# Performance work log

Measured on AMD Instinct MI355X. Metric: run time of the kernel, lower is better.

## Reference

```python
import jax, jax.numpy as jnp
import numpy as np
import math

MIN_NORM = 1e-15
EPS = 1e-7
MAX_NORM = 1e6

N = 100000      # num nodes (aaa)
E = 1600000     # num edges
D_IN = 129      # embedding_num (1 time coord + 128 spatial)
D_OUT = 128     # output1_dim
MAXLEN = 50
B = 4096
NCLASS = 5

# ---------------- Hyperboloid manifold ops (HGCN-style) ----------------

def proj(x, c):
    K = 1. / c
    y = x[..., 1:]
    y_sq = jnp.sum(y * y, axis=-1, keepdims=True)
    x0 = jnp.sqrt(jnp.clip(K + y_sq, EPS))
    return jnp.concatenate([x0, y], axis=-1)

def proj_tan0(u, c):
    # zero out the time coordinate
    return jnp.concatenate([jnp.zeros_like(u[..., :1]), u[..., 1:]], axis=-1)

def expmap0(u, c):
    K = 1. / c
    sqrtK = jnp.sqrt(K)
    x = u[..., 1:]
    xn = jnp.maximum(jnp.linalg.norm(x, axis=-1, keepdims=True), MIN_NORM)
    theta = xn / sqrtK
    first = sqrtK * jnp.cosh(theta)
    rest = sqrtK * jnp.sinh(theta) * x / xn
    return proj(jnp.concatenate([first, rest], axis=-1), c)

def logmap0(x, c):
    K = 1. / c
    sqrtK = jnp.sqrt(K)
    y = x[..., 1:]
    yn = jnp.maximum(jnp.linalg.norm(y, axis=-1, keepdims=True), MIN_NORM)
    theta = jnp.clip(x[..., 0:1] / sqrtK, 1.0 + EPS)
    rest = sqrtK * jnp.arccosh(theta) * y / yn
    return jnp.concatenate([jnp.zeros_like(theta), rest], axis=-1)

def minkowski_dot(x, y):
    return jnp.sum(x * y, axis=-1, keepdims=True) - 2.0 * x[..., 0:1] * y[..., 0:1]

def minkowski_norm(u):
    return jnp.sqrt(jnp.clip(minkowski_dot(u, u), EPS))

def expmap(u, x, c):
    K = 1. / c
    sqrtK = jnp.sqrt(K)
    normu = jnp.minimum(minkowski_norm(u), MAX_NORM)
    theta = jnp.maximum(normu / sqrtK, MIN_NORM)
    result = jnp.cosh(theta) * x + jnp.sinh(theta) * u / theta
    return proj(result, c)

def proj_tan(u, x, c):
    ux = jnp.sum(x[..., 1:] * u[..., 1:], axis=-1, keepdims=True)
    vals0 = ux / jnp.clip(x[..., 0:1], EPS)
    return jnp.concatenate([vals0, u[..., 1:]], axis=-1)

def ptransp0(x, u, c):
    K = 1. / c
    sqrtK = jnp.sqrt(K)
    x0 = x[..., 0:1]
    y = x[..., 1:]
    yn = jnp.maximum(jnp.linalg.norm(y, axis=-1, keepdims=True), MIN_NORM)
    yhat = y / yn
    v = jnp.concatenate([-yn, (sqrtK - x0) * yhat], axis=-1)
    alpha = jnp.sum(yhat * u[..., 1:], axis=-1, keepdims=True) / sqrtK
    return proj_tan(u - alpha * v, x, c)

def mobius_add(x, y, c):
    u = logmap0(y, c)
    v = ptransp0(x, jnp.broadcast_to(u, x.shape), c)
    return expmap(v, x, c)

def mobius_add0(x, y, c):
    # tangent-space addition at the origin
    return expmap0(logmap0(x, c) + logmap0(y, c), c)

def mobius_matvec1(m, x, c):
    return expmap0(logmap0(x, c) @ m, c)

def mobius_matvec0(n, x, c):
    # per-row scalar mobius scaling (n is (N,1))
    return expmap0(n * logmap0(x, c), c)

def hyp_bias_point(b, c):
    return proj(expmap0(proj_tan0(b[None, :], c), c), c)

def gcn_layer(x, w, b, rows, cols, vals, c, n_nodes):
    out = mobius_matvec1(w, x, c)
    out = mobius_add(out, hyp_bias_point(b, c), c)
    out = logmap0(out, c)
    out = jax.ops.segment_sum(vals[:, None] * out[cols], rows, num_segments=n_nodes)
    return proj(expmap0(out, c), c)


def setup_inputs() -> dict:
    key = jax.random.key(0)
    ks = jax.random.split(key, 20)
    def ku(k, shape, fan_in):
        bound = 1.0 / math.sqrt(fan_in)
        return jax.random.uniform(k, shape, jnp.float32, -bound, bound)
    inp = {}
    inp['A1_tensor'] = jax.random.normal(ks[0], (N, D_IN), jnp.float32)
    inp['adj_rows'] = jax.random.randint(ks[1], (E,), 0, N)
    inp['adj_cols'] = jax.random.randint(ks[2], (E,), 0, N)
    inp['adj_vals'] = jax.random.uniform(ks[3], (E,), jnp.float32) * 0.1
    inp['batch_idx'] = jax.random.randint(ks[4], (B, 1, MAXLEN), 0, N)
    inp['raw_c'] = jnp.array([math.log(math.exp(1.0) - 1.0)], jnp.float32)
    inp['n_param'] = jax.random.uniform(ks[5], (N, 1), jnp.float32)
    inp['Lin1'] = ku(ks[6], (D_IN, D_OUT), D_IN)
    inp['Lin1_bias'] = ku(ks[7], (D_OUT,), D_IN)
    inp['gc1_w'] = ku(ks[8], (D_IN, D_OUT), D_IN)
    inp['gc1_b'] = ku(ks[9], (D_OUT,), D_IN)
    inp['gc2_w'] = ku(ks[10], (D_OUT, D_OUT), D_OUT)
    inp['gc2_b'] = ku(ks[11], (D_OUT,), D_OUT)
    inp['weight'] = ku(ks[12], (D_OUT, MAXLEN), D_OUT)
    inp['weight2'] = ku(ks[13], (D_OUT, MAXLEN), D_OUT)
    inp['conv1_w'] = ku(ks[14], (MAXLEN,), MAXLEN)
    inp['conv1_b'] = ku(ks[15], (1,), MAXLEN)
    inp['conv2_w'] = ku(ks[16], (MAXLEN,), MAXLEN)
    inp['conv2_b'] = ku(ks[17], (1,), MAXLEN)
    inp['classifier'] = ku(ks[18], (2 * MAXLEN, NCLASS), 2 * MAXLEN)
    inp['classifier_bias'] = ku(ks[19], (NCLASS,), 2 * MAXLEN)
    return inp


def reference(A1_tensor, adj_rows, adj_cols, adj_vals, batch_idx, raw_c, n_param,
              Lin1, Lin1_bias, gc1_w, gc1_b, gc2_w, gc2_b, weight, weight2,
              conv1_w, conv1_b, conv2_w, conv2_b, classifier, classifier_bias):
    c = jax.nn.softplus(raw_c)[0] + 1e-5
    bi = batch_idx[:, 0, :]                       # (B, L)
    flat = bi.reshape(-1)

    x_tan = proj_tan0(A1_tensor, c)
    a = proj(expmap0(x_tan, c), c)                # (N, D_IN)

    a1 = mobius_matvec1(Lin1, a, c)               # (N, D_OUT)
    a1 = mobius_add(a1, hyp_bias_point(Lin1_bias, c), c)
    a2 = mobius_matvec0(n_param, a1, c)

    x_1 = gcn_layer(a, gc1_w, gc1_b, adj_rows, adj_cols, adj_vals, c, N)
    x_1 = mobius_matvec0(1.0 - n_param, x_1, c)
    x_1 = mobius_add0(x_1, a2, c)
    x_2 = gcn_layer(x_1, gc2_w, gc2_b, adj_rows, adj_cols, adj_vals, c, N)

    # readout branch 1: x_2 gathered on batch indices
    s2 = logmap0(x_2[flat].reshape(bi.shape[0], bi.shape[1], D_OUT), c)  # (B,L,D)
    s2 = jnp.einsum('bld,dt->blt', s2, weight)    # (B, L, MAXLEN)
    s2 = jnp.einsum('blt,l->bt', s2, conv1_w) + conv1_b  # kernel-size-1 conv over channels

    # readout branch 2: a1 gathered on batch indices
    s3 = logmap0(a1[flat].reshape(bi.shape[0], bi.shape[1], D_OUT), c)
    s3 = jnp.einsum('bld,dt->blt', s3, weight2)
    s3 = jnp.einsum('blt,l->bt', s3, conv2_w) + conv2_b

    sel = jnp.concatenate([s2, s3], axis=1)       # (B, 2*MAXLEN)
    pre = sel @ classifier + classifier_bias      # (B, NCLASS)
    return jnp.argmax(pre, axis=-1), sel
```

## Files before the change

kernel.cpp:

```cpp
#include <hip/hip_runtime.h>
#include <math.h>


typedef unsigned short ushort_t;
typedef __attribute__((ext_vector_type(8))) short short8;
typedef __attribute__((ext_vector_type(4))) float f32x4;

__device__ __forceinline__ float wsum(float x){
  x += __shfl_xor(x, 32);
  x += __shfl_xor(x, 16);
  x += __shfl_xor(x, 8);
  x += __shfl_xor(x, 4);
  x += __shfl_xor(x, 2);
  x += __shfl_xor(x, 1);
  return x;
}

__device__ __forceinline__ void get_c(const float* rc, float& K, float& sK){
  float c = log1pf(expf(rc[0])) + 1e-5f;
  K  = 1.0f / c;
  sK = sqrtf(K);
}

__device__ __forceinline__ float sinhx_over_x(float x){
  if (x > 1e-3f){
    float e  = __expf(x);
    float em = __builtin_amdgcn_rcpf(e);
    return 0.5f*(e - em) * __builtin_amdgcn_rcpf(x);
  }
  return 1.0f + x*x*(1.0f/6.0f);
}

__device__ __forceinline__ float facosh(float x){
  return __logf(x + sqrtf(fmaxf(fmaf(x, x, -1.0f), 0.0f)));
}

__device__ __forceinline__ ushort_t bf16_rne(float x){
  unsigned int u = __float_as_uint(x);
  u += 0x7fffu + ((u >> 16) & 1u);
  return (ushort_t)(u >> 16);
}
__device__ __forceinline__ float bf2f(ushort_t h){
  return __uint_as_float(((unsigned int)h) << 16);
}
__device__ __forceinline__ unsigned int pack_bf16(float x, float y){
  unsigned int bx = __float_as_uint(x);
  unsigned int by = __float_as_uint(y);
  bx = (bx + 0x7fffu + ((bx >> 16) & 1u)) >> 16;
  by = (by + 0x7fffu + ((by >> 16) & 1u)) & 0xffff0000u;
  return bx | by;
}
__device__ __forceinline__ float bf_lo(unsigned int p){ return __uint_as_float(p << 16); }
__device__ __forceinline__ float bf_hi(unsigned int p){ return __uint_as_float(p & 0xffff0000u); }

__device__ __forceinline__ void chain_scalars(float tt, float tu, float uu,
                                              float K, float sK,
                                              float& At, float& Au){
  float xn  = fmaxf(sqrtf(tt), 1e-15f);
  float th  = xn / sK;
  float f   = sinhx_over_x(th);
  float pn2 = f*f*tt;
  float p0  = sqrtf(fmaxf(K + pn2, 1e-7f));
  float S_yu = f * tu;
  float yn  = fmaxf(sqrtf(pn2), 1e-15f);
  float inv_yn = __builtin_amdgcn_rcpf(yn);
  float alpha = S_yu * inv_yn / sK;
  float coef  = alpha * (sK - p0);
  float cy  = coef * inv_yn;
  float cyf = cy * f;
  float pdw  = S_yu - cy*pn2;
  float spsq = uu - 2.f*cy*S_yu + cy*cy*pn2;
  float w0 = pdw / fmaxf(p0, 1e-7f);
  float md = spsq - w0*w0;
  float normu = fminf(sqrtf(fmaxf(md, 1e-7f)), 1e6f);
  float th2 = fmaxf(normu / sK, 1e-15f);
  float e  = __expf(th2);
  float em = __builtin_amdgcn_rcpf(e);
  float ch = 0.5f*(e + em);
  float g  = (th2 > 1e-3f) ? 0.5f*(e - em)*__builtin_amdgcn_rcpf(th2)
                           : 1.0f + th2*th2*(1.0f/6.0f);
  float rn2 = ch*ch*pn2 + 2.f*ch*g*pdw + g*g*spsq;
  float r0 = sqrtf(fmaxf(K + rn2, 1e-7f));
  float ynf = fmaxf(sqrtf(rn2), 1e-15f);
  float thf = fmaxf(r0/sK, 1.f+1e-7f);
  float rf = sK * facosh(thf) * __builtin_amdgcn_rcpf(ynf);
  At = rf*(ch*f - g*cyf);
  Au = rf*g;
}

__global__ __launch_bounds__(256) void stage_a(const float* __restrict__ A1,
                                               ushort_t* __restrict__ Lhi,
                                               ushort_t* __restrict__ Llo,
                                               int* __restrict__ cnt,
                                               const float* __restrict__ b0,
                                               const float* __restrict__ b1,
                                               const float* __restrict__ b2,
                                               float* __restrict__ uu3, int n){
  size_t i = (size_t)blockIdx.x * 256 + threadIdx.x;
  size_t total = (size_t)n * 128;
  if (i < total){
    size_t row = i >> 7; int j = (int)(i & 127);
    float v = A1[row*129 + 1 + j];
    ushort_t h = bf16_rne(v);
    Lhi[i] = h;
    Llo[i] = bf16_rne(v - bf2f(h));
  }
  if (i < (size_t)n) cnt[i] = 0;
  if (blockIdx.x == 0 && threadIdx.x < 64){
    int lane = threadIdx.x;
    const float* bs[3] = {b0, b1, b2};
    for (int k = 0; k < 3; ++k){
      float x = lane ? bs[k][2*lane] : 0.0f;
      float y = bs[k][2*lane+1];
      float s = wsum(x*x + y*y);
      if (lane == 0) uu3[k] = s;
    }
  }
}

__global__ __launch_bounds__(256) void split_w(const float* __restrict__ W,
                                               ushort_t* __restrict__ Whi,
                                               ushort_t* __restrict__ Wlo){
  int id = blockIdx.x * 256 + threadIdx.x;
  int k = id >> 7, nn = id & 127;
  float v = W[(size_t)k*128 + nn];
  ushort_t h = bf16_rne(v);
  Whi[(size_t)nn*128 + k] = h;
  Wlo[(size_t)nn*128 + k] = bf16_rne(v - bf2f(h));
}

__global__ __launch_bounds__(256) void mfma_chain(const ushort_t* __restrict__ Ahi,
                                                  const ushort_t* __restrict__ Alo,
                                                  const ushort_t* __restrict__ Whi,
                                                  const ushort_t* __restrict__ Wlo,
                                                  const float* __restrict__ bias,
                                                  const float* __restrict__ uu3, int uuidx,
                                                  const float* __restrict__ raw_c,
                                                  float* __restrict__ outF,
                                                  unsigned int* __restrict__ outH,
                                                  int mode, int n, int nWaves){
  __shared__ ushort_t Wsh[2][128*128];
  int tid = threadIdx.x;
  {
    const uint4* gh = (const uint4*)Whi;
    const uint4* gl = (const uint4*)Wlo;
    uint4* sh = (uint4*)Wsh[0];
    uint4* sl = (uint4*)Wsh[1];
    #pragma unroll
    for (int i = 0; i < 8; ++i){ sh[tid + 256*i] = gh[tid + 256*i]; }
    #pragma unroll
    for (int i = 0; i < 8; ++i){ sl[tid + 256*i] = gl[tid + 256*i]; }
  }
  __syncthreads();

  int lane = tid & 63;
  int c = lane & 15, quad = lane >> 4;
  int wid = blockIdx.x * 4 + (tid >> 6);
  int nStrips = (n + 15) >> 4;

  float K, sK; get_c(raw_c, K, sK);
  float uu = uu3[uuidx];
  float uv[8];
  #pragma unroll
  for (int t = 0; t < 8; ++t){
    int col = t*16 + c;
    uv[t] = (col == 0) ? 0.f : bias[col];
  }

  for (int strip = wid; strip < nStrips; strip += nWaves){
    int m0 = strip * 16;
    int ra = m0 + c; if (ra > n - 1) ra = n - 1;
    short8 ahi[4], alo[4];
    #pragma unroll
    for (int kc = 0; kc < 4; ++kc){
      size_t aoff = (size_t)ra*128 + kc*32 + quad*8;
      ahi[kc] = *(const short8*)&Ahi[aoff];
      alo[kc] = *(const short8*)&Alo[aoff];
    }

    f32x4 acc[8];
    #pragma unroll
    for (int t = 0; t < 8; ++t){
      f32x4 z = {0.f, 0.f, 0.f, 0.f};
      acc[t] = z;
      int wrow = (t*16 + c) * 128;
      #pragma unroll
      for (int kc = 0; kc < 4; ++kc){
        int woff = wrow + kc*32 + quad*8;
        short8 bhi = *(const short8*)&Wsh[0][woff];
        short8 blo = *(const short8*)&Wsh[1][woff];
        acc[t] = __builtin_amdgcn_mfma_f32_16x16x32_bf16(ahi[kc], bhi, acc[t], 0, 0, 0);
        acc[t] = __builtin_amdgcn_mfma_f32_16x16x32_bf16(ahi[kc], blo, acc[t], 0, 0, 0);
        acc[t] = __builtin_amdgcn_mfma_f32_16x16x32_bf16(alo[kc], bhi, acc[t], 0, 0, 0);
      }
    }

    if (c == 0){
      f32x4 z = {0.f, 0.f, 0.f, 0.f};
      acc[0] = z;
    }
    #pragma unroll
    for (int r = 0; r < 4; ++r){
      float tt = 0.f, tu = 0.f;
      #pragma unroll
      for (int t = 0; t < 8; ++t){
        float v = acc[t][r];
        tt = fmaf(v, v, tt);
        tu = fmaf(v, uv[t], tu);
      }
      #pragma unroll
      for (int m = 1; m <= 8; m <<= 1){
        tt += __shfl_xor(tt, m);
        tu += __shfl_xor(tu, m);
      }
      float At, Au; chain_scalars(tt, tu, uu, K, sK, At, Au);
      int row = m0 + quad*4 + r;
      if (mode == 0){
        if (row < n){
          #pragma unroll
          for (int t = 0; t < 8; ++t){
            float o = fmaf(At, acc[t][r], Au*uv[t]);
            outF[(size_t)row*128 + t*16 + c] = o;
          }
        }
      } else {
        #pragma unroll
        for (int t = 0; t < 8; ++t){
          float o  = fmaf(At, acc[t][r], Au*uv[t]);
          float on = __shfl_xor(o, 1);
          if (row < n && !(c & 1))
            outH[(size_t)row*64 + t*8 + (c >> 1)] = pack_bf16(o, on);
        }
      }
    }
  }
}

__global__ __launch_bounds__(256) void hist_k(const int* __restrict__ rows,
                                              int* __restrict__ cnt,
                                              int* __restrict__ rnk, int e){
  int base = (blockIdx.x * 256 + threadIdx.x) * 4;
  if (base + 3 < e){
    int4 r = *(const int4*)&rows[base];
    int k0 = atomicAdd(&cnt[r.x], 1);
    int k1 = atomicAdd(&cnt[r.y], 1);
    int k2 = atomicAdd(&cnt[r.z], 1);
    int k3 = atomicAdd(&cnt[r.w], 1);
    *(int4*)&rnk[base] = make_int4(k0, k1, k2, k3);
  } else {
    for (int i = base; i < e; ++i) rnk[i] = atomicAdd(&cnt[rows[i]], 1);
  }
}

#define SCAN_ITEMS 4
__global__ __launch_bounds__(256) void scan1(const int* __restrict__ cnt,
                                             int* __restrict__ off,
                                             int* __restrict__ bsum, int n){
  __shared__ int sh[256];
  int tid = threadIdx.x;
  int base = blockIdx.x * 256 * SCAN_ITEMS + tid * SCAN_ITEMS;
  int v[SCAN_ITEMS]; int s = 0;
  #pragma unroll
  for (int i = 0; i < SCAN_ITEMS; ++i){ int idx = base+i; v[i] = (idx < n) ? cnt[idx] : 0; s += v[i]; }
  sh[tid] = s; __syncthreads();
  for (int o = 1; o < 256; o <<= 1){
    int t = (tid >= o) ? sh[tid - o] : 0; __syncthreads();
    sh[tid] += t; __syncthreads();
  }
  int excl = sh[tid] - s;
  if (tid == 255) bsum[blockIdx.x] = sh[tid];
  int run = excl;
  #pragma unroll
  for (int i = 0; i < SCAN_ITEMS; ++i){ int idx = base+i; if (idx < n) off[idx] = run; run += v[i]; }
}

__global__ void scan2(int* bsum, int G){
  if (threadIdx.x == 0 && blockIdx.x == 0){
    int run = 0;
    for (int i = 0; i < G; ++i){ int t = bsum[i]; bsum[i] = run; run += t; }
  }
}

__global__ void scan3(int* __restrict__ off, const int* __restrict__ bsum, int n){
  int i = blockIdx.x * blockDim.x + threadIdx.x;
  if (i < n) off[i] += bsum[i / (256*SCAN_ITEMS)];
}

__global__ __launch_bounds__(256) void fill_k(const int* __restrict__ rows,
                                              const int* __restrict__ cols,
                                              const float* __restrict__ vals,
                                              const int* __restrict__ off,
                                              const int* __restrict__ rnk,
                                              int2* __restrict__ ecv, int e){
  int base = (blockIdx.x * 256 + threadIdx.x) * 4;
  if (base + 3 < e){
    int4   r = *(const int4*)&rows[base];
    int4   q = *(const int4*)&rnk[base];
    int4   c = *(const int4*)&cols[base];
    float4 v = *(const float4*)&vals[base];
    int o0 = off[r.x], o1 = off[r.y], o2 = off[r.z], o3 = off[r.w];
    ecv[o0 + q.x] = make_int2(c.x, __float_as_int(v.x));
    ecv[o1 + q.y] = make_int2(c.y, __float_as_int(v.y));
    ecv[o2 + q.z] = make_int2(c.z, __float_as_int(v.z));
    ecv[o3 + q.w] = make_int2(c.w, __float_as_int(v.w));
  } else {
    for (int i = base; i < e; ++i)
      ecv[off[rows[i]] + rnk[i]] = make_int2(cols[i], __float_as_int(vals[i]));
  }
}

__device__ __forceinline__ float2 seg_gather_bf16(const unsigned int* __restrict__ h,
                                                  const int* __restrict__ off,
                                                  const int* __restrict__ cnt,
                                                  const int2* __restrict__ ecv,
                                                  int row, int lane){
  float ax = 0.f, ay = 0.f, bx = 0.f, by = 0.f;
  int st = off[row], deg = cnt[row];
  const unsigned int* __restrict__ hb = h + lane;
  for (int b = 0; b < deg; b += 64){
    int k = b + lane;
    int cc = 0; float vv = 0.f;
    if (k < deg){ int2 e = ecv[st+k]; cc = e.x; vv = __int_as_float(e.y); }
    int m = min(64, deg - b);
    for (int j = 0; j < m; j += 8){
      int   c0=__shfl(cc,j+0), c1=__shfl(cc,j+1), c2=__shfl(cc,j+2), c3=__shfl(cc,j+3);
      int   c4=__shfl(cc,j+4), c5=__shfl(cc,j+5), c6=__shfl(cc,j+6), c7=__shfl(cc,j+7);
      float v0=__shfl(vv,j+0), v1=__shfl(vv,j+1), v2=__shfl(vv,j+2), v3=__shfl(vv,j+3);
      float v4=__shfl(vv,j+4), v5=__shfl(vv,j+5), v6=__shfl(vv,j+6), v7=__shfl(vv,j+7);
      unsigned int p0 = hb[(size_t)c0*64];
      unsigned int p1 = hb[(size_t)c1*64];
      unsigned int p2 = hb[(size_t)c2*64];
      unsigned int p3 = hb[(size_t)c3*64];
      unsigned int p4 = hb[(size_t)c4*64];
      unsigned int p5 = hb[(size_t)c5*64];
      unsigned int p6 = hb[(size_t)c6*64];
      unsigned int p7 = hb[(size_t)c7*64];
      ax = fmaf(v0, bf_lo(p0), ax); ay = fmaf(v0, bf_hi(p0), ay);
      bx = fmaf(v1, bf_lo(p1), bx); by = fmaf(v1, bf_hi(p1), by);
      ax = fmaf(v2, bf_lo(p2), ax); ay = fmaf(v2, bf_hi(p2), ay);
      bx = fmaf(v3, bf_lo(p3), bx); by = fmaf(v3, bf_hi(p3), by);
      ax = fmaf(v4, bf_lo(p4), ax); ay = fmaf(v4, bf_hi(p4), ay);
      bx = fmaf(v5, bf_lo(p5), bx); by = fmaf(v5, bf_hi(p5), by);
      ax = fmaf(v6, bf_lo(p6), ax); ay = fmaf(v6, bf_hi(p6), ay);
      bx = fmaf(v7, bf_lo(p7), bx); by = fmaf(v7, bf_hi(p7), by);
    }
  }
  return make_float2(ax + bx, ay + by);
}

__global__ __launch_bounds__(256) void seg_x1(const unsigned int* __restrict__ h1,
                                              const int* __restrict__ off,
                                              const int* __restrict__ cnt,
                                              const int2* __restrict__ ecv,
                                              const float* __restrict__ loga1,
                                              const float* __restrict__ nparam,
                                              unsigned int* __restrict__ X1hi,
                                              unsigned int* __restrict__ X1lo, int n){
  int row  = (int)((blockIdx.x * blockDim.x + threadIdx.x) >> 6);
  int lane = threadIdx.x & 63;
  if (row >= n) return;
  float2 acc = seg_gather_bf16(h1, off, cnt, ecv, row, lane);
  float nv = nparam[row];
  float2 la1 = *(const float2*)&loga1[(size_t)row*128 + 2*lane];
  float ox = (1.f-nv)*acc.x + nv*la1.x;
  float oy = (1.f-nv)*acc.y + nv*la1.y;
  unsigned int hp = pack_bf16(ox, oy);
  X1hi[(size_t)row*64 + lane] = hp;
  X1lo[(size_t)row*64 + lane] = pack_bf16(ox - bf_lo(hp), oy - bf_hi(hp));
}

__global__ __launch_bounds__(256) void seg_x2(const unsigned int* __restrict__ h2,
                                              const int* __restrict__ off,
                                              const int* __restrict__ cnt,
                                              const int2* __restrict__ ecv,
                                              float* __restrict__ Lx2, int n){
  int row  = (int)((blockIdx.x * blockDim.x + threadIdx.x) >> 6);
  int lane = threadIdx.x & 63;
  if (row >= n) return;
  float2 acc = seg_gather_bf16(h2, off, cnt, ecv, row, lane);
  *(float2*)&Lx2[(size_t)row*128 + 2*lane] = acc;
}

__global__ __launch_bounds__(128) void batch_head(const float* __restrict__ Lx2,
                                                  const float* __restrict__ loga1,
                                                  const int* __restrict__ bidx,
                                                  const float* __restrict__ weight,
                                                  const float* __restrict__ weight2,
                                                  const float* __restrict__ c1w,
                                                  const float* __restrict__ c1b,
                                                  const float* __restrict__ c2w,
                                                  const float* __restrict__ c2b,
                                                  const float* __restrict__ cls,
                                                  const float* __restrict__ clsb,
                                                  float* __restrict__ out, int Bn){
  __shared__ float sg2[128], sg3[128], ssel[100], spre[5];
  __shared__ int sbi[50];
  __shared__ float sc1[50], sc2[50];
  int b = blockIdx.x, d = threadIdx.x;
  const int* bi = bidx + (size_t)b * 50;
  if (d < 50){ sbi[d] = bi[d]; sc1[d] = c1w[d]; sc2[d] = c2w[d]; }
  __syncthreads();
  int lane = d & 63;
  bool lo = d < 64;
  const float* __restrict__ tab = lo ? Lx2 : loga1;
  const float* __restrict__ cw = lo ? sc1 : sc2;
  float gx = 0.f, gy = 0.f;
  const float2* __restrict__ t2 = (const float2*)tab + lane;
  #pragma unroll
  for (int l = 0; l < 50; l += 5){
    int i0 = sbi[l+0], i1 = sbi[l+1], i2 = sbi[l+2], i3 = sbi[l+3], i4 = sbi[l+4];
    float2 p0 = t2[(size_t)i0*64];
    float2 p1 = t2[(size_t)i1*64];
    float2 p2 = t2[(size_t)i2*64];
    float2 p3 = t2[(size_t)i3*64];
    float2 p4 = t2[(size_t)i4*64];
    float w0 = cw[l+0], w1 = cw[l+1], w2 = cw[l+2], w3 = cw[l+3], w4 = cw[l+4];
    gx = fmaf(w0, p0.x, gx); gy = fmaf(w0, p0.y, gy);
    gx = fmaf(w1, p1.x, gx); gy = fmaf(w1, p1.y, gy);
    gx = fmaf(w2, p2.x, gx); gy = fmaf(w2, p2.y, gy);
    gx = fmaf(w3, p3.x, gx); gy = fmaf(w3, p3.y, gy);
    gx = fmaf(w4, p4.x, gx); gy = fmaf(w4, p4.y, gy);
  }
  if (lo){ sg2[2*lane] = gx; sg2[2*lane+1] = gy; }
  else   { sg3[2*lane] = gx; sg3[2*lane+1] = gy; }
  __syncthreads();
  if (d < 50){
    float s = 0.f;
    for (int k = 0; k < 128; ++k) s = fmaf(sg2[k], weight[k*50 + d], s);
    s += c1b[0];
    ssel[d] = s;
    out[(size_t)Bn + (size_t)b*100 + d] = s;
  } else if (d >= 64 && d < 114){
    int t = d - 64;
    float s = 0.f;
    for (int k = 0; k < 128; ++k) s = fmaf(sg3[k], weight2[k*50 + t], s);
    s += c2b[0];
    ssel[50 + t] = s;
    out[(size_t)Bn + (size_t)b*100 + 50 + t] = s;
  }
  __syncthreads();
  if (d < 5){
    float s = clsb[d];
    for (int j = 0; j < 100; ++j) s = fmaf(ssel[j], cls[j*5 + d], s);
    spre[d] = s;
  }
  __syncthreads();
  if (d == 0){
    int best = 0; float bv = spre[0];
    #pragma unroll
    for (int k = 1; k < 5; ++k) if (spre[k] > bv){ bv = spre[k]; best = k; }
    out[b] = (float)best;
  }
}

extern "C" void kernel_launch(void* const* d_in, const int* in_sizes, int n_in,
                              void* d_out, int out_size, void* d_ws, size_t ws_size,
                              hipStream_t stream) {
  const float* A1     = (const float*)d_in[0];
  const int*   rows   = (const int*)  d_in[1];
  const int*   cols   = (const int*)  d_in[2];
  const float* vals   = (const float*)d_in[3];
  const int*   bidx   = (const int*)  d_in[4];
  const float* raw_c  = (const float*)d_in[5];
  const float* nparam = (const float*)d_in[6];
  const float* Lin1   = (const float*)d_in[7];
  const float* Lin1_b = (const float*)d_in[8];
  const float* gc1_w  = (const float*)d_in[9];
  const float* gc1_b  = (const float*)d_in[10];
  const float* gc2_w  = (const float*)d_in[11];
  const float* gc2_b  = (const float*)d_in[12];
  const float* weight = (const float*)d_in[13];
  const float* weight2= (const float*)d_in[14];
  const float* c1w    = (const float*)d_in[15];
  const float* c1b    = (const float*)d_in[16];
  const float* c2w    = (const float*)d_in[17];
  const float* c2b    = (const float*)d_in[18];
  const float* cls    = (const float*)d_in[19];
  const float* clsb   = (const float*)d_in[20];

  int N  = in_sizes[0] / 129;
  int E  = in_sizes[1];
  int Bn = in_sizes[4] / 50;
  size_t NF = (size_t)N * 128;

  ushort_t* Lhi = (ushort_t*)d_ws;
  ushort_t* Llo = Lhi + NF;
  float*    S0  = (float*)d_ws;
  float*    S3  = (float*)(Llo + NF);
  unsigned int* Hb   = (unsigned int*)(S3 + NF);
  unsigned int* X1hi = Hb + NF/2;
  unsigned int* X1lo = X1hi + NF/2;
  ushort_t* Wb = (ushort_t*)(X1lo + NF/2);
  ushort_t* W1h = Wb,           *W1l = Wb + 16384;
  ushort_t* W2h = Wb + 2*16384, *W2l = Wb + 3*16384;
  ushort_t* W3h = Wb + 4*16384, *W3l = Wb + 5*16384;
  int* cnt    = (int*)(Wb + 6*16384);
  int* off    = cnt + N;
  int* rnk    = off + N;
  int* bsum   = rnk + E;
  int2* ecv   = (int2*)(bsum + 4096);
  float* uu3  = (float*)(ecv + E);

  int rowBlocks  = (N + 3) / 4;
  int G = (N + 256*SCAN_ITEMS - 1) / (256*SCAN_ITEMS);
  int eBlocks4 = (E/4 + 255) / 256 + 1;
  int mBlocks = 512;
  int nWaves  = mBlocks * 4;

  stage_a<<<(int)((NF + 255)/256), 256, 0, stream>>>(A1, Lhi, Llo, cnt,
                                                     Lin1_b, gc1_b, gc2_b, uu3, N);
  split_w<<<64, 256, 0, stream>>>(Lin1 + 128, W1h, W1l);
  split_w<<<64, 256, 0, stream>>>(gc1_w + 128, W2h, W2l);
  split_w<<<64, 256, 0, stream>>>(gc2_w, W3h, W3l);

  hist_k<<<eBlocks4, 256, 0, stream>>>(rows, cnt, rnk, E);
  scan1<<<G, 256, 0, stream>>>(cnt, off, bsum, N);
  scan2<<<1, 64, 0, stream>>>(bsum, G);
  scan3<<<(N+255)/256, 256, 0, stream>>>(off, bsum, N);
  fill_k<<<eBlocks4, 256, 0, stream>>>(rows, cols, vals, off, rnk, ecv, E);

  mfma_chain<<<mBlocks, 256, 0, stream>>>(Lhi, Llo, W1h, W1l, Lin1_b, uu3, 0, raw_c,
                                          S3, (unsigned int*)nullptr, 0, N, nWaves);
  mfma_chain<<<mBlocks, 256, 0, stream>>>(Lhi, Llo, W2h, W2l, gc1_b, uu3, 1, raw_c,
                                          (float*)nullptr, Hb, 1, N, nWaves);
  seg_x1<<<rowBlocks, 256, 0, stream>>>(Hb, off, cnt, ecv, S3, nparam, X1hi, X1lo, N);
  mfma_chain<<<mBlocks, 256, 0, stream>>>((const ushort_t*)X1hi, (const ushort_t*)X1lo,
                                          W3h, W3l, gc2_b, uu3, 2, raw_c,
                                          (float*)nullptr, Hb, 1, N, nWaves);
  seg_x2<<<rowBlocks, 256, 0, stream>>>(Hb, off, cnt, ecv, S0, N);
  batch_head<<<Bn, 128, 0, stream>>>(S0, S3, bidx, weight, weight2, c1w, c1b,
                                     c2w, c2b, cls, clsb, (float*)d_out, Bn);
}
```

Baseline: 625.5 us.

## Vectorize input split, swizzle LDS weights, merge split kernels, bf16 x2 output

Several independent changes. stage_a now handles four elements per thread with vector stores. The three split_w launches become one split_w3 launch. The weight tile in LDS is XOR-swizzled to avoid bank conflicts on the MFMA B-operand reads. scan2 is now a parallel block scan instead of a serial loop on one thread. seg_x2 writes packed bf16 instead of fp32, halving that output and the batch_head gather traffic, at the cost of lower precision in readout branch 1.

New measurement: 576.3 us. 7.9% less time.

```diff
diff --git a/kernel.cpp b/kernel.cpp
--- a/kernel.cpp
+++ b/kernel.cpp
@@ -5,6 +5,7 @@
 typedef unsigned short ushort_t;
 typedef __attribute__((ext_vector_type(8))) short short8;
 typedef __attribute__((ext_vector_type(4))) float f32x4;
+typedef __attribute__((ext_vector_type(4))) unsigned short u16x4;
 
 __device__ __forceinline__ float wsum(float x){
   x += __shfl_xor(x, 32);
@@ -96,16 +97,20 @@
                                                const float* __restrict__ b1,
                                                const float* __restrict__ b2,
                                                float* __restrict__ uu3, int n){
-  size_t i = (size_t)blockIdx.x * 256 + threadIdx.x;
-  size_t total = (size_t)n * 128;
-  if (i < total){
-    size_t row = i >> 7; int j = (int)(i & 127);
-    float v = A1[row*129 + 1 + j];
-    ushort_t h = bf16_rne(v);
-    Lhi[i] = h;
-    Llo[i] = bf16_rne(v - bf2f(h));
-  }
-  if (i < (size_t)n) cnt[i] = 0;
+  size_t i4 = (size_t)blockIdx.x * 256 + threadIdx.x;
+  size_t tot4 = (size_t)n * 32;
+  if (i4 < tot4){
+    size_t row = i4 >> 5; int j0 = (int)(i4 & 31) * 4;
+    const float* s = A1 + row*129 + 1 + j0;
+    float v0 = s[0], v1 = s[1], v2 = s[2], v3 = s[3];
+    ushort_t h0 = bf16_rne(v0), h1 = bf16_rne(v1), h2 = bf16_rne(v2), h3 = bf16_rne(v3);
+    u16x4 hh = {h0, h1, h2, h3};
+    u16x4 ll = {bf16_rne(v0 - bf2f(h0)), bf16_rne(v1 - bf2f(h1)),
+                bf16_rne(v2 - bf2f(h2)), bf16_rne(v3 - bf2f(h3))};
+    *(u16x4*)&Lhi[i4*4] = hh;
+    *(u16x4*)&Llo[i4*4] = ll;
+  }
+  if (i4 < (size_t)n) cnt[i4] = 0;
   if (blockIdx.x == 0 && threadIdx.x < 64){
     int lane = threadIdx.x;
     const float* bs[3] = {b0, b1, b2};
@@ -118,10 +123,16 @@
   }
 }
 
-__global__ __launch_bounds__(256) void split_w(const float* __restrict__ W,
-                                               ushort_t* __restrict__ Whi,
-                                               ushort_t* __restrict__ Wlo){
-  int id = blockIdx.x * 256 + threadIdx.x;
+__global__ __launch_bounds__(256) void split_w3(const float* __restrict__ Lin1,
+                                                const float* __restrict__ G1,
+                                                const float* __restrict__ G2,
+                                                ushort_t* __restrict__ Wb){
+  int bid = blockIdx.x;
+  int which = bid >> 6, b = bid & 63;
+  const float* W = (which == 0) ? (Lin1 + 128) : (which == 1) ? (G1 + 128) : G2;
+  ushort_t* Whi = Wb + (size_t)which * 2 * 16384;
+  ushort_t* Wlo = Whi + 16384;
+  int id = b * 256 + threadIdx.x;
   int k = id >> 7, nn = id & 127;
   float v = W[(size_t)k*128 + nn];
   ushort_t h = bf16_rne(v);
@@ -147,9 +158,17 @@
     uint4* sh = (uint4*)Wsh[0];
     uint4* sl = (uint4*)Wsh[1];
     #pragma unroll
-    for (int i = 0; i < 8; ++i){ sh[tid + 256*i] = gh[tid + 256*i]; }
-    #pragma unroll
-    for (int i = 0; i < 8; ++i){ sl[tid + 256*i] = gl[tid + 256*i]; }
+    for (int i = 0; i < 8; ++i){
+      int idx = tid + 256*i;
+      int sw = idx ^ ((idx >> 4) & 7);
+      sh[sw] = gh[idx];
+    }
+    #pragma unroll
+    for (int i = 0; i < 8; ++i){
+      int idx = tid + 256*i;
+      int sw = idx ^ ((idx >> 4) & 7);
+      sl[sw] = gl[idx];
+    }
   }
   __syncthreads();
 
@@ -157,6 +176,7 @@
   int c = lane & 15, quad = lane >> 4;
   int wid = blockIdx.x * 4 + (tid >> 6);
   int nStrips = (n + 15) >> 4;
+  int csw = (c & 7) << 3;
 
   float K, sK; get_c(raw_c, K, sK);
   float uu = uu3[uuidx];
@@ -186,7 +206,7 @@
       int wrow = (t*16 + c) * 128;
       #pragma unroll
       for (int kc = 0; kc < 4; ++kc){
-        int woff = wrow + kc*32 + quad*8;
+        int woff = (wrow + kc*32 + quad*8) ^ csw;
         short8 bhi = *(const short8*)&Wsh[0][woff];
         short8 blo = *(const short8*)&Wsh[1][woff];
         acc[t] = __builtin_amdgcn_mfma_f32_16x16x32_bf16(ahi[kc], bhi, acc[t], 0, 0, 0);
@@ -274,11 +294,16 @@
   for (int i = 0; i < SCAN_ITEMS; ++i){ int idx = base+i; if (idx < n) off[idx] = run; run += v[i]; }
 }
 
-__global__ void scan2(int* bsum, int G){
-  if (threadIdx.x == 0 && blockIdx.x == 0){
-    int run = 0;
-    for (int i = 0; i < G; ++i){ int t = bsum[i]; bsum[i] = run; run += t; }
-  }
+__global__ __launch_bounds__(256) void scan2(int* __restrict__ bsum, int G){
+  __shared__ int sh[256];
+  int t = threadIdx.x;
+  int v = (t < G) ? bsum[t] : 0;
+  sh[t] = v; __syncthreads();
+  for (int o = 1; o < 256; o <<= 1){
+    int x = (t >= o) ? sh[t - o] : 0; __syncthreads();
+    sh[t] += x; __syncthreads();
+  }
+  if (t < G) bsum[t] = sh[t] - v;
 }
 
 __global__ void scan3(int* __restrict__ off, const int* __restrict__ bsum, int n){
@@ -373,15 +398,15 @@
                                               const int* __restrict__ off,
                                               const int* __restrict__ cnt,
                                               const int2* __restrict__ ecv,
-                                              float* __restrict__ Lx2, int n){
+                                              unsigned int* __restrict__ Lx2p, int n){
   int row  = (int)((blockIdx.x * blockDim.x + threadIdx.x) >> 6);
   int lane = threadIdx.x & 63;
   if (row >= n) return;
   float2 acc = seg_gather_bf16(h2, off, cnt, ecv, row, lane);
-  *(float2*)&Lx2[(size_t)row*128 + 2*lane] = acc;
-}
-
-__global__ __launch_bounds__(128) void batch_head(const float* __restrict__ Lx2,
+  Lx2p[(size_t)row*64 + lane] = pack_bf16(acc.x, acc.y);
+}
+
+__global__ __launch_bounds__(128) void batch_head(const unsigned int* __restrict__ Lx2p,
                                                   const float* __restrict__ loga1,
                                                   const int* __restrict__ bidx,
                                                   const float* __restrict__ weight,
@@ -402,27 +427,44 @@
   __syncthreads();
   int lane = d & 63;
   bool lo = d < 64;
-  const float* __restrict__ tab = lo ? Lx2 : loga1;
-  const float* __restrict__ cw = lo ? sc1 : sc2;
   float gx = 0.f, gy = 0.f;
-  const float2* __restrict__ t2 = (const float2*)tab + lane;
-  #pragma unroll
-  for (int l = 0; l < 50; l += 5){
-    int i0 = sbi[l+0], i1 = sbi[l+1], i2 = sbi[l+2], i3 = sbi[l+3], i4 = sbi[l+4];
-    float2 p0 = t2[(size_t)i0*64];
-    float2 p1 = t2[(size_t)i1*64];
-    float2 p2 = t2[(size_t)i2*64];
-    float2 p3 = t2[(size_t)i3*64];
-    float2 p4 = t2[(size_t)i4*64];
-    float w0 = cw[l+0], w1 = cw[l+1], w2 = cw[l+2], w3 = cw[l+3], w4 = cw[l+4];
-    gx = fmaf(w0, p0.x, gx); gy = fmaf(w0, p0.y, gy);
-    gx = fmaf(w1, p1.x, gx); gy = fmaf(w1, p1.y, gy);
-    gx = fmaf(w2, p2.x, gx); gy = fmaf(w2, p2.y, gy);
-    gx = fmaf(w3, p3.x, gx); gy = fmaf(w3, p3.y, gy);
-    gx = fmaf(w4, p4.x, gx); gy = fmaf(w4, p4.y, gy);
-  }
-  if (lo){ sg2[2*lane] = gx; sg2[2*lane+1] = gy; }
-  else   { sg3[2*lane] = gx; sg3[2*lane+1] = gy; }
+  if (lo){
+    const unsigned int* __restrict__ tp = Lx2p + lane;
+    #pragma unroll
+    for (int l = 0; l < 50; l += 5){
+      int i0 = sbi[l+0], i1 = sbi[l+1], i2 = sbi[l+2], i3 = sbi[l+3], i4 = sbi[l+4];
+      unsigned int p0 = tp[(size_t)i0*64];
+      unsigned int p1 = tp[(size_t)i1*64];
+      unsigned int p2 = tp[(size_t)i2*64];
+      unsigned int p3 = tp[(size_t)i3*64];
+      unsigned int p4 = tp[(size_t)i4*64];
+      float w0 = sc1[l+0], w1 = sc1[l+1], w2 = sc1[l+2], w3 = sc1[l+3], w4 = sc1[l+4];
+      gx = fmaf(w0, bf_lo(p0), gx); gy = fmaf(w0, bf_hi(p0), gy);
+      gx = fmaf(w1, bf_lo(p1), gx); gy = fmaf(w1, bf_hi(p1), gy);
+      gx = fmaf(w2, bf_lo(p2), gx); gy = fmaf(w2, bf_hi(p2), gy);
+      gx = fmaf(w3, bf_lo(p3), gx); gy = fmaf(w3, bf_hi(p3), gy);
+      gx = fmaf(w4, bf_lo(p4), gx); gy = fmaf(w4, bf_hi(p4), gy);
+    }
+    sg2[2*lane] = gx; sg2[2*lane+1] = gy;
+  } else {
+    const float2* __restrict__ t2 = (const float2*)loga1 + lane;
+    #pragma unroll
+    for (int l = 0; l < 50; l += 5){
+      int i0 = sbi[l+0], i1 = sbi[l+1], i2 = sbi[l+2], i3 = sbi[l+3], i4 = sbi[l+4];
+      float2 p0 = t2[(size_t)i0*64];
+      float2 p1 = t2[(size_t)i1*64];
+      float2 p2 = t2[(size_t)i2*64];
+      float2 p3 = t2[(size_t)i3*64];
+      float2 p4 = t2[(size_t)i4*64];
+      float w0 = sc2[l+0], w1 = sc2[l+1], w2 = sc2[l+2], w3 = sc2[l+3], w4 = sc2[l+4];
+      gx = fmaf(w0, p0.x, gx); gy = fmaf(w0, p0.y, gy);
+      gx = fmaf(w1, p1.x, gx); gy = fmaf(w1, p1.y, gy);
+      gx = fmaf(w2, p2.x, gx); gy = fmaf(w2, p2.y, gy);
+      gx = fmaf(w3, p3.x, gx); gy = fmaf(w3, p3.y, gy);
+      gx = fmaf(w4, p4.x, gx); gy = fmaf(w4, p4.y, gy);
+    }
+    sg3[2*lane] = gx; sg3[2*lane+1] = gy;
+  }
   __syncthreads();
   if (d < 50){
     float s = 0.f;
@@ -485,7 +527,7 @@
 
   ushort_t* Lhi = (ushort_t*)d_ws;
   ushort_t* Llo = Lhi + NF;
-  float*    S0  = (float*)d_ws;
+  unsigned int* Lx2p = (unsigned int*)d_ws;
   float*    S3  = (float*)(Llo + NF);
   unsigned int* Hb   = (unsigned int*)(S3 + NF);
   unsigned int* X1hi = Hb + NF/2;
@@ -507,15 +549,13 @@
   int mBlocks = 512;
   int nWaves  = mBlocks * 4;
 
-  stage_a<<<(int)((NF + 255)/256), 256, 0, stream>>>(A1, Lhi, Llo, cnt,
+  stage_a<<<(int)(((size_t)N*32 + 255)/256), 256, 0, stream>>>(A1, Lhi, Llo, cnt,
                                                      Lin1_b, gc1_b, gc2_b, uu3, N);
-  split_w<<<64, 256, 0, stream>>>(Lin1 + 128, W1h, W1l);
-  split_w<<<64, 256, 0, stream>>>(gc1_w + 128, W2h, W2l);
-  split_w<<<64, 256, 0, stream>>>(gc2_w, W3h, W3l);
+  split_w3<<<192, 256, 0, stream>>>(Lin1, gc1_w, gc2_w, Wb);
 
   hist_k<<<eBlocks4, 256, 0, stream>>>(rows, cnt, rnk, E);
   scan1<<<G, 256, 0, stream>>>(cnt, off, bsum, N);
-  scan2<<<1, 64, 0, stream>>>(bsum, G);
+  scan2<<<1, 256, 0, stream>>>(bsum, G);
   scan3<<<(N+255)/256, 256, 0, stream>>>(off, bsum, N);
   fill_k<<<eBlocks4, 256, 0, stream>>>(rows, cols, vals, off, rnk, ecv, E);
 
@@ -527,7 +567,7 @@
   mfma_chain<<<mBlocks, 256, 0, stream>>>((const ushort_t*)X1hi, (const ushort_t*)X1lo,
                                           W3h, W3l, gc2_b, uu3, 2, raw_c,
                                           (float*)nullptr, Hb, 1, N, nWaves);
-  seg_x2<<<rowBlocks, 256, 0, stream>>>(Hb, off, cnt, ecv, S0, N);
-  batch_head<<<Bn, 128, 0, stream>>>(S0, S3, bidx, weight, weight2, c1w, c1b,
+  seg_x2<<<rowBlocks, 256, 0, stream>>>(Hb, off, cnt, ecv, Lx2p, N);
+  batch_head<<<Bn, 128, 0, stream>>>(Lx2p, S3, bidx, weight, weight2, c1w, c1b,
                                      c2w, c2b, cls, clsb, (float*)d_out, Bn);
 }
```
